# Performance work log

Measured on AMD Instinct MI355X. Metric: run time of the kernel, lower is better.

## Reference

```python
import jax, jax.numpy as jnp
import numpy as np

DIM = 1024
HEADS = 16

def setup_inputs() -> dict:
    key = jax.random.key(0)
    k1, k2, k3, k4 = jax.random.split(key, 4)
    x = jax.random.normal(k1, (2, 2048, DIM), dtype=jnp.float32)
    ln_gamma = jnp.ones((DIM,), dtype=jnp.float32)
    ln_beta = jnp.zeros((DIM,), dtype=jnp.float32)
    # torch Linear weight is [out, in]; store transposed [in, out] for x @ W
    W_qkv = jax.random.normal(k2, (DIM, 3 * DIM), dtype=jnp.float32) * (DIM ** -0.5)
    W_out = jax.random.normal(k3, (DIM, DIM), dtype=jnp.float32) * (DIM ** -0.5)
    b_out = jax.random.normal(k4, (DIM,), dtype=jnp.float32) * 0.02
    return {"x": x, "ln_gamma": ln_gamma, "ln_beta": ln_beta,
            "W_qkv": W_qkv, "W_out": W_out, "b_out": b_out}

def reference(x, ln_gamma, ln_beta, W_qkv, W_out, b_out):
    B, N, C = x.shape
    H = HEADS
    Dh = C // H
    scale = Dh ** -0.5
    # LayerNorm (eps=1e-5, torch default)
    mu = jnp.mean(x, axis=-1, keepdims=True)
    var = jnp.var(x, axis=-1, keepdims=True)
    xn = (x - mu) / jnp.sqrt(var + 1e-5) * ln_gamma + ln_beta
    # QKV projection: [B,N,3C] -> [3,B,H,N,Dh]
    qkv = (xn @ W_qkv).reshape(B, N, 3, H, Dh).transpose(2, 0, 3, 1, 4)
    q, k, v = qkv[0], qkv[1], qkv[2]
    attn = jnp.einsum('bhnd,bhmd->bhnm', q, k) * scale  # [B,H,N,N]
    attn = jax.nn.softmax(attn, axis=-1)
    out = jnp.einsum('bhnm,bhmd->bhnd', attn, v)  # [B,H,N,Dh]
    out = out.transpose(0, 2, 1, 3).reshape(B, N, C)
    return out @ W_out + b_out
```

## Files before the change

kernel.cpp:

```cpp
#include <hip/hip_runtime.h>
#include <hip/hip_bf16.h>

#define DIM 1024
#define HEADS 16
#define DH 64
#define SEQ 2048
#define BATCH 2
#define ROWS (BATCH*SEQ)
#define C3 (3*DIM)
#define NT (SEQ/64)

typedef __attribute__((ext_vector_type(8))) short s16x8;
typedef __attribute__((ext_vector_type(4))) short s16x4;
typedef __attribute__((ext_vector_type(4))) float f32x4;
typedef __attribute__((ext_vector_type(16))) float f32x16;
typedef __attribute__((ext_vector_type(4))) unsigned int u32x4;
typedef __attribute__((ext_vector_type(2))) unsigned int u32x2;

__device__ __forceinline__ void gll16(const void* g, void* l) {
  __builtin_amdgcn_global_load_lds((const __attribute__((address_space(1))) void*)g,
                                   (__attribute__((address_space(3))) void*)l, 16, 0, 0);
}
__device__ __forceinline__ float bf2f(short s) {
  return __builtin_bit_cast(float, ((unsigned)(unsigned short)s) << 16);
}
__device__ __forceinline__ short f2bf(float f) {
  return (short)__bfloat16_as_ushort(__float2bfloat16(f));
}
__device__ __forceinline__ unsigned pk2(float a, float b) {
  unsigned lo = (unsigned)__bfloat16_as_ushort(__float2bfloat16(a));
  unsigned hh = (unsigned)__bfloat16_as_ushort(__float2bfloat16(b));
  return lo | (hh << 16);
}
__device__ __forceinline__ float fexp2(float x) {
#if __has_builtin(__builtin_amdgcn_exp2f)
  return __builtin_amdgcn_exp2f(x);
#else
  float r; asm("v_exp_f32 %0, %1" : "=v"(r) : "v"(x)); return r;
#endif
}

__global__ __launch_bounds__(256) void prep_kernel(const float* __restrict__ x,
    const float* __restrict__ gamma, const float* __restrict__ beta,
    __hip_bfloat16* __restrict__ xn,
    const float* __restrict__ Wqkv, __hip_bfloat16* __restrict__ wqkv_t,
    const float* __restrict__ Wout, __hip_bfloat16* __restrict__ wout_t) {
  const int bid = blockIdx.x;
  const int t = threadIdx.x;
  if (bid < ROWS) {
    __shared__ float red[8];
    const float4* xp = (const float4*)(x + (size_t)bid * DIM);
    float4 v = xp[t];
    float s = v.x + v.y + v.z + v.w;
    float q = v.x*v.x + v.y*v.y + v.z*v.z + v.w*v.w;
    for (int off = 32; off >= 1; off >>= 1) {
      s += __shfl_xor(s, off, 64);
      q += __shfl_xor(q, off, 64);
    }
    int w = t >> 6;
    if ((t & 63) == 0) { red[w] = s; red[4 + w] = q; }
    __syncthreads();
    s = red[0] + red[1] + red[2] + red[3];
    q = red[4] + red[5] + red[6] + red[7];
    float mu = s * (1.0f / DIM);
    float var = q * (1.0f / DIM) - mu * mu;
    float rstd = rsqrtf(var + 1e-5f);
    float4 g4 = ((const float4*)gamma)[t];
    float4 b4 = ((const float4*)beta)[t];
    __hip_bfloat16* op = xn + (size_t)bid * DIM + t * 4;
    op[0] = __float2bfloat16((v.x - mu) * rstd * g4.x + b4.x);
    op[1] = __float2bfloat16((v.y - mu) * rstd * g4.y + b4.y);
    op[2] = __float2bfloat16((v.z - mu) * rstd * g4.z + b4.z);
    op[3] = __float2bfloat16((v.w - mu) * rstd * g4.w + b4.w);
  } else {
    __shared__ float tile[32][33];
    const float* in; __hip_bfloat16* out; int R, Cn, c0, r0;
    if (bid < ROWS + 3072) {
      int id = bid - ROWS;
      in = Wqkv; out = wqkv_t; R = DIM; Cn = C3;
      c0 = (id % 96) * 32; r0 = (id / 96) * 32;
    } else {
      int id = bid - ROWS - 3072;
      in = Wout; out = wout_t; R = DIM; Cn = DIM;
      c0 = (id % 32) * 32; r0 = (id / 32) * 32;
    }
    int tx = t & 31, ty = t >> 5;
#pragma unroll
    for (int i = 0; i < 4; i++)
      tile[ty + i * 8][tx] = in[(size_t)(r0 + ty + i * 8) * Cn + c0 + tx];
    __syncthreads();
#pragma unroll
    for (int i = 0; i < 4; i++)
      out[(size_t)(c0 + ty + i * 8) * R + r0 + tx] = __float2bfloat16(tile[tx][ty + i * 8]);
  }
}

__global__ __launch_bounds__(512) void gemm192(const __hip_bfloat16* __restrict__ A,
    const __hip_bfloat16* __restrict__ Bt, __hip_bfloat16* __restrict__ C,
    int M, int Nc, int K) {
  __shared__ short lds_a[2][256 * 64];
  __shared__ short lds_b[2][192 * 64];
  const int t = threadIdx.x, l = t & 63;
  const int w = t >> 6, wr = w >> 2, wc = w & 3;
  const int m0 = blockIdx.y * 256, n0 = blockIdx.x * 192;
  const short* Ab = (const short*)A;
  const short* Bb = (const short*)Bt;
  f32x4 acc[8][3] = {};
  const int srow = t >> 3;
  const int schk = (t & 7) ^ (srow & 7);
  const int NIT = K / 64;

  {
    char* la = (char*)&lds_a[0][0];
    char* lb = (char*)&lds_b[0][0];
#pragma unroll
    for (int p = 0; p < 4; p++)
      gll16(Ab + (size_t)(m0 + p * 64 + srow) * K + schk * 8, la + p * 8192 + t * 16);
#pragma unroll
    for (int p = 0; p < 3; p++)
      gll16(Bb + (size_t)(n0 + p * 64 + srow) * K + schk * 8, lb + p * 8192 + t * 16);
  }
  for (int it = 0; it < NIT; ++it) {
    const int cur = it & 1;
    __syncthreads();
    if (it + 1 < NIT) {
      const int kk = (it + 1) * 64;
      char* la = (char*)&lds_a[cur ^ 1][0];
      char* lb = (char*)&lds_b[cur ^ 1][0];
#pragma unroll
      for (int p = 0; p < 4; p++)
        gll16(Ab + (size_t)(m0 + p * 64 + srow) * K + kk + schk * 8, la + p * 8192 + t * 16);
#pragma unroll
      for (int p = 0; p < 3; p++)
        gll16(Bb + (size_t)(n0 + p * 64 + srow) * K + kk + schk * 8, lb + p * 8192 + t * 16);
      asm volatile("s_waitcnt vmcnt(7)" ::: "memory");
    } else {
      asm volatile("s_waitcnt vmcnt(0)" ::: "memory");
    }
    __syncthreads();
    const char* la = (const char*)&lds_a[cur][0];
    const char* lb = (const char*)&lds_b[cur][0];
    s16x8 af[4], bf[3];
#define GPH_READ_A(FH, S)                                                     \
    _Pragma("unroll")                                                         \
    for (int f = 0; f < 4; f++) {                                             \
      int row = wr * 128 + (FH * 4 + f) * 16 + (l & 15);                      \
      int chk = (((S) * 4 + (l >> 4)) ^ (l & 7)) * 16;                        \
      af[f] = *(const s16x8*)(la + row * 128 + chk);                          \
    }
#define GPH_READ_B(S)                                                         \
    _Pragma("unroll")                                                         \
    for (int n = 0; n < 3; n++) {                                             \
      int row = wc * 48 + n * 16 + (l & 15);                                  \
      int chk = (((S) * 4 + (l >> 4)) ^ (l & 7)) * 16;                        \
      bf[n] = *(const s16x8*)(lb + row * 128 + chk);                          \
    }
#define GPH_MFMA(FH)                                                          \
    __builtin_amdgcn_s_barrier();                                             \
    asm volatile("s_waitcnt lgkmcnt(0)" ::: "memory");                        \
    __builtin_amdgcn_sched_barrier(0);                                        \
    __builtin_amdgcn_s_setprio(1);                                            \
    _Pragma("unroll")                                                         \
    for (int f = 0; f < 4; f++)                                               \
      _Pragma("unroll")                                                       \
      for (int n = 0; n < 3; n++)                                             \
        acc[FH * 4 + f][n] =                                                  \
            __builtin_amdgcn_mfma_f32_16x16x32_bf16(af[f], bf[n],             \
                                                    acc[FH * 4 + f][n], 0, 0, 0); \
    __builtin_amdgcn_s_setprio(0);                                            \
    __builtin_amdgcn_s_barrier();

    GPH_READ_A(0, 0) GPH_READ_B(0) GPH_MFMA(0)
    GPH_READ_A(1, 0) GPH_MFMA(1)
    GPH_READ_A(0, 1) GPH_READ_B(1) GPH_MFMA(0)
    GPH_READ_A(1, 1) GPH_MFMA(1)
#undef GPH_READ_A
#undef GPH_READ_B
#undef GPH_MFMA
  }
#pragma unroll
  for (int f = 0; f < 8; f++)
#pragma unroll
    for (int n = 0; n < 3; n++) {
      int col = n0 + wc * 48 + n * 16 + (l & 15);
#pragma unroll
      for (int r = 0; r < 4; r++) {
        int row = m0 + wr * 128 + f * 16 + (l >> 4) * 4 + r;
        C[(size_t)row * Nc + col] = __float2bfloat16(acc[f][n][r]);
      }
    }
}

__global__ __launch_bounds__(256) void gemm_out(const __hip_bfloat16* __restrict__ A,
    const __hip_bfloat16* __restrict__ Bt, float* __restrict__ C,
    const float* __restrict__ bias) {
  __shared__ short lds_a[2][128 * 32];
  __shared__ short lds_b[2][64 * 32];
  const int t = threadIdx.x, l = t & 63, w = t >> 6;
  const int wr = w >> 1, wc = w & 1;
  const int m0 = blockIdx.y * 128, n0 = blockIdx.x * 64;
  const short* Ab = (const short*)A;
  const short* Bb = (const short*)Bt;
  const int K = DIM;
  f32x4 acc[4][2] = {};
  const int srow = t >> 2, scol = (t & 3) * 8;
  {
    char* la = (char*)&lds_a[0][0];
    char* lb = (char*)&lds_b[0][0];
    gll16(Ab + (size_t)(m0 + srow) * K + scol,      la + t * 16);
    gll16(Ab + (size_t)(m0 + 64 + srow) * K + scol, la + 4096 + t * 16);
    gll16(Bb + (size_t)(n0 + srow) * K + scol,      lb + t * 16);
  }
  for (int it = 0; it < K / 32; ++it) {
    const int cur = it & 1;
    __syncthreads();
    if (it + 1 < K / 32) {
      const int kk = (it + 1) * 32;
      char* la = (char*)&lds_a[cur ^ 1][0];
      char* lb = (char*)&lds_b[cur ^ 1][0];
      gll16(Ab + (size_t)(m0 + srow) * K + kk + scol,      la + t * 16);
      gll16(Ab + (size_t)(m0 + 64 + srow) * K + kk + scol, la + 4096 + t * 16);
      gll16(Bb + (size_t)(n0 + srow) * K + kk + scol,      lb + t * 16);
      asm volatile("s_waitcnt vmcnt(3)" ::: "memory");
    } else {
      asm volatile("s_waitcnt vmcnt(0)" ::: "memory");
    }
    __syncthreads();
    s16x8 af[4], bf[2];
#pragma unroll
    for (int m = 0; m < 4; m++)
      af[m] = *(const s16x8*)&lds_a[cur][(wr * 64 + m * 16 + (l & 15)) * 32 + (l >> 4) * 8];
#pragma unroll
    for (int n = 0; n < 2; n++)
      bf[n] = *(const s16x8*)&lds_b[cur][(wc * 32 + n * 16 + (l & 15)) * 32 + (l >> 4) * 8];
#pragma unroll
    for (int m = 0; m < 4; m++)
#pragma unroll
      for (int n = 0; n < 2; n++)
        acc[m][n] = __builtin_amdgcn_mfma_f32_16x16x32_bf16(af[m], bf[n], acc[m][n], 0, 0, 0);
  }
#pragma unroll
  for (int m = 0; m < 4; m++)
#pragma unroll
    for (int n = 0; n < 2; n++) {
      int col = n0 + wc * 32 + n * 16 + (l & 15);
      float bb = bias[col];
#pragma unroll
      for (int r = 0; r < 4; r++) {
        int row = m0 + wr * 64 + m * 16 + (l >> 4) * 4 + r;
        C[(size_t)row * DIM + col] = acc[m][n][r] + bb;
      }
    }
}

__global__ __launch_bounds__(512) void attn_kernel(const __hip_bfloat16* __restrict__ qkv,
    __hip_bfloat16* __restrict__ attno) {
  const int t = threadIdx.x, l = t & 63, w = t >> 6;
  const int hi = l >> 5, lq = l & 31;
  const int bid = blockIdx.x;
  const int xcd = bid & 7, j = bid >> 3;
  const int bh = xcd + 8 * (j & 3);
  const int qb = j >> 2;
  const int b = bh >> 4, h = bh & 15;
  const short* base  = (const short*)qkv + (size_t)b * SEQ * C3 + h * DH;
  const short* kbase = base + DIM;
  const short* vbase = base + 2 * DIM;
  const int qr0 = qb * 256 + w * 32;

  __shared__ short kbuf[2][2][64 * 64];
  __shared__ short vbuf[2][2][64 * 64];

  const float SCL = 0.125f * 1.44269504089f;
  s16x8 qf[4];
#pragma unroll
  for (int dk = 0; dk < 4; dk++) {
    s16x8 raw = *(const s16x8*)(base + (size_t)(qr0 + lq) * C3 + dk * 16 + hi * 8);
#pragma unroll
    for (int j2 = 0; j2 < 8; j2++) qf[dk][j2] = f2bf(bf2f(raw[j2]) * SCL);
  }

  s16x8 ones;
#pragma unroll
  for (int j2 = 0; j2 < 8; j2++) ones[j2] = (short)0x3F80;

  f32x16 o0, o1, osum, zf;
#pragma unroll
  for (int r = 0; r < 16; r++) { o0[r] = 0.f; o1[r] = 0.f; osum[r] = 0.f; zf[r] = 0.f; }
  asm volatile("" : "+v"(zf));

  const int krow = t >> 3;
  const int ksrc = (t & 7) ^ (krow & 7);
  const int vr = t & 31, vcg = t >> 5;

#define V_LOAD(VA, VB, ROW0)                                                    \
  VA = __builtin_bit_cast(u32x2, *(const s16x4*)(vbase + (size_t)((ROW0) + 2 * vr) * C3 + vcg * 4)); \
  VB = __builtin_bit_cast(u32x2, *(const s16x4*)(vbase + (size_t)((ROW0) + 2 * vr + 1) * C3 + vcg * 4));

#define V_WRITE(VD, VA, VB)                                                     \
  { char* vd_ = (char*)(VD);                                                    \
    _Pragma("unroll")                                                           \
    for (int i = 0; i < 4; i++) {                                               \
      int d = vcg * 4 + i;                                                      \
      unsigned dw = __builtin_amdgcn_perm((VB)[i >> 1], (VA)[i >> 1],           \
                                          (i & 1) ? 0x07060302u : 0x05040100u); \
      *(unsigned*)(vd_ + d * 128 + (((vr >> 2) ^ (d & 7)) * 16) + (vr & 3) * 4) = dw; } }

  {
    gll16(kbase + (size_t)krow * C3 + ksrc * 8,        (char*)&kbuf[0][0][0] + t * 16);
    gll16(kbase + (size_t)(64 + krow) * C3 + ksrc * 8, (char*)&kbuf[0][1][0] + t * 16);
    u32x2 va0, vb0, va1, vb1;
    V_LOAD(va0, vb0, 0)
    V_LOAD(va1, vb1, 64)
    V_WRITE(&vbuf[0][0][0], va0, vb0)
    V_WRITE(&vbuf[0][1][0], va1, vb1)
  }
  __syncthreads();

#define ATTN_SUB(KB, VB)                                                        \
  {                                                                             \
    const char* kb_ = (const char*)(KB);                                        \
    const char* vbp_ = (const char*)(VB);                                       \
    f32x16 st0, st1;                                                            \
    { int chk0 = (hi ^ (l & 7)) * 16;                                           \
      s16x8 kf0 = *(const s16x8*)(kb_ + (size_t)lq * 128 + chk0);               \
      s16x8 kf1 = *(const s16x8*)(kb_ + (size_t)(32 + lq) * 128 + chk0);        \
      st0 = __builtin_amdgcn_mfma_f32_32x32x16_bf16(kf0, qf[0], zf, 0, 0, 0);   \
      st1 = __builtin_amdgcn_mfma_f32_32x32x16_bf16(kf1, qf[0], zf, 0, 0, 0); } \
    _Pragma("unroll")                                                           \
    for (int dk = 1; dk < 4; dk++) {                                            \
      int chk = ((2 * dk + hi) ^ (l & 7)) * 16;                                 \
      s16x8 kf0 = *(const s16x8*)(kb_ + (size_t)lq * 128 + chk);                \
      s16x8 kf1 = *(const s16x8*)(kb_ + (size_t)(32 + lq) * 128 + chk);         \
      st0 = __builtin_amdgcn_mfma_f32_32x32x16_bf16(kf0, qf[dk], st0, 0, 0, 0); \
      st1 = __builtin_amdgcn_mfma_f32_32x32x16_bf16(kf1, qf[dk], st1, 0, 0, 0); \
    }                                                                           \
    _Pragma("unroll")                                                           \
    for (int r = 0; r < 16; r++) { st0[r] = fexp2(st0[r]); st1[r] = fexp2(st1[r]); } \
    _Pragma("unroll")                                                           \
    for (int n = 0; n < 2; n++) {                                               \
      const f32x16& stn = n ? st1 : st0;                                        \
      _Pragma("unroll")                                                         \
      for (int ksl = 0; ksl < 2; ksl++) {                                       \
        int rb = ksl * 8;                                                       \
        int a_ = (int)pk2(stn[rb + 0], stn[rb + 1]);                            \
        int b_ = (int)pk2(stn[rb + 2], stn[rb + 3]);                            \
        int c_ = (int)pk2(stn[rb + 4], stn[rb + 5]);                            \
        int d_ = (int)pk2(stn[rb + 6], stn[rb + 7]);                            \
        asm volatile("v_permlane32_swap_b32 %0, %1" : "+v"(a_), "+v"(c_));      \
        asm volatile("v_permlane32_swap_b32 %0, %1" : "+v"(b_), "+v"(d_));      \
        u32x4 fr;                                                               \
        fr.x = (unsigned)a_;  fr.y = (unsigned)b_;                              \
        fr.z = (unsigned)c_;  fr.w = (unsigned)d_;                              \
        s16x8 pa = __builtin_bit_cast(s16x8, fr);                               \
        int ks = n * 2 + ksl;                                                   \
        int chk = ((2 * ks + hi) ^ (l & 7)) * 16;                               \
        s16x8 vf0 = *(const s16x8*)(vbp_ + (size_t)lq * 128 + chk);             \
        s16x8 vf1 = *(const s16x8*)(vbp_ + (size_t)(32 + lq) * 128 + chk);      \
        o0   = __builtin_amdgcn_mfma_f32_32x32x16_bf16(pa, vf0, o0, 0, 0, 0);   \
        o1   = __builtin_amdgcn_mfma_f32_32x32x16_bf16(pa, vf1, o1, 0, 0, 0);   \
        osum = __builtin_amdgcn_mfma_f32_32x32x16_bf16(pa, ones, osum, 0, 0, 0);\
      }                                                                         \
    }                                                                           \
  }

  for (int it = 0; it < NT / 2; ++it) {
    const int cur = it & 1;
    const bool pf = (it + 1 < NT / 2);
    u32x2 va0, vb0, va1, vb1;
    if (pf) {
      const int kv1 = (it + 1) * 128;
      gll16(kbase + (size_t)(kv1 + krow) * C3 + ksrc * 8,      (char*)&kbuf[cur ^ 1][0][0] + t * 16);
      gll16(kbase + (size_t)(kv1 + 64 + krow) * C3 + ksrc * 8, (char*)&kbuf[cur ^ 1][1][0] + t * 16);
      V_LOAD(va0, vb0, kv1)
      V_LOAD(va1, vb1, kv1 + 64)
    }
    ATTN_SUB(&kbuf[cur][0][0], &vbuf[cur][0][0])
    ATTN_SUB(&kbuf[cur][1][0], &vbuf[cur][1][0])
    if (pf) {
      V_WRITE(&vbuf[cur ^ 1][0][0], va0, vb0)
      V_WRITE(&vbuf[cur ^ 1][1][0], va1, vb1)
    }
    __syncthreads();
  }
#undef ATTN_SUB
#undef V_LOAD
#undef V_WRITE

#pragma unroll
  for (int r = 0; r < 16; r++) {
    int qr = (r & 3) + 8 * (r >> 2) + 4 * hi;
    float ir = 1.0f / osum[r];
    size_t rowoff = (size_t)(b * SEQ + qr0 + qr) * DIM + h * DH;
    attno[rowoff + lq]      = __float2bfloat16(o0[r] * ir);
    attno[rowoff + 32 + lq] = __float2bfloat16(o1[r] * ir);
  }
}

extern "C" void kernel_launch(void* const* d_in, const int* in_sizes, int n_in,
                              void* d_out, int out_size, void* d_ws, size_t ws_size,
                              hipStream_t stream) {
  const float* x     = (const float*)d_in[0];
  const float* gamma = (const float*)d_in[1];
  const float* beta  = (const float*)d_in[2];
  const float* Wqkv  = (const float*)d_in[3];
  const float* Wout  = (const float*)d_in[4];
  const float* bout  = (const float*)d_in[5];

  __hip_bfloat16* xn     = (__hip_bfloat16*)d_ws;
  __hip_bfloat16* wqkv_t = xn + (size_t)ROWS * DIM;
  __hip_bfloat16* wout_t = wqkv_t + (size_t)C3 * DIM;
  __hip_bfloat16* qkv    = wout_t + (size_t)DIM * DIM;
  __hip_bfloat16* attno  = qkv + (size_t)ROWS * C3;

  prep_kernel<<<ROWS + 3072 + 1024, 256, 0, stream>>>(x, gamma, beta, xn,
                                                      Wqkv, wqkv_t, Wout, wout_t);
  gemm192<<<dim3(C3 / 192, ROWS / 256), 512, 0, stream>>>(xn, wqkv_t, qkv, ROWS, C3, DIM);
  attn_kernel<<<SEQ / 256 * BATCH * HEADS, 512, 0, stream>>>(qkv, attno);
  gemm_out<<<dim3(DIM / 64, ROWS / 128), 256, 0, stream>>>(attno, wout_t, (float*)d_out, bout);
}
```

Baseline: 119.8 us.

## Use 32x32 MFMA tiles in QKV GEMM and halve attention block size

The QKV GEMM switches from 16x16x32 to 32x32x16 MFMA with a 4x2 wave layout where each wave covers 64x96, so fewer LDS fragment reads are needed per FLOP. The attention kernel moves to 256-thread blocks covering 128 query rows, launching twice as many blocks, with wider 16-byte V loads and a K staging macro adjusted to the new thread count. The aim is to cut LDS traffic in the GEMM and improve occupancy and load balance in attention. The cost is more K/V staging per query row, since each KV tile is now shared by fewer queries.

```diff
diff --git a/kernel.cpp b/kernel.cpp
--- a/kernel.cpp
+++ b/kernel.cpp
@@ -101,11 +101,12 @@
   __shared__ short lds_a[2][256 * 64];
   __shared__ short lds_b[2][192 * 64];
   const int t = threadIdx.x, l = t & 63;
-  const int w = t >> 6, wr = w >> 2, wc = w & 3;
+  const int w = t >> 6, wr = w >> 1, wc = w & 1;
+  const int hi = l >> 5;
   const int m0 = blockIdx.y * 256, n0 = blockIdx.x * 192;
   const short* Ab = (const short*)A;
   const short* Bb = (const short*)Bt;
-  f32x4 acc[8][3] = {};
+  f32x16 acc[2][3] = {};
   const int srow = t >> 3;
   const int schk = (t & 7) ^ (srow & 7);
   const int NIT = K / 64;
@@ -140,53 +141,45 @@
     __syncthreads();
     const char* la = (const char*)&lds_a[cur][0];
     const char* lb = (const char*)&lds_b[cur][0];
-    s16x8 af[4], bf[3];
-#define GPH_READ_A(FH, S)                                                     \
-    _Pragma("unroll")                                                         \
-    for (int f = 0; f < 4; f++) {                                             \
-      int row = wr * 128 + (FH * 4 + f) * 16 + (l & 15);                      \
-      int chk = (((S) * 4 + (l >> 4)) ^ (l & 7)) * 16;                        \
-      af[f] = *(const s16x8*)(la + row * 128 + chk);                          \
-    }
-#define GPH_READ_B(S)                                                         \
-    _Pragma("unroll")                                                         \
-    for (int n = 0; n < 3; n++) {                                             \
-      int row = wc * 48 + n * 16 + (l & 15);                                  \
-      int chk = (((S) * 4 + (l >> 4)) ^ (l & 7)) * 16;                        \
-      bf[n] = *(const s16x8*)(lb + row * 128 + chk);                          \
-    }
-#define GPH_MFMA(FH)                                                          \
-    __builtin_amdgcn_s_barrier();                                             \
-    asm volatile("s_waitcnt lgkmcnt(0)" ::: "memory");                        \
-    __builtin_amdgcn_sched_barrier(0);                                        \
-    __builtin_amdgcn_s_setprio(1);                                            \
-    _Pragma("unroll")                                                         \
-    for (int f = 0; f < 4; f++)                                               \
-      _Pragma("unroll")                                                       \
-      for (int n = 0; n < 3; n++)                                             \
-        acc[FH * 4 + f][n] =                                                  \
-            __builtin_amdgcn_mfma_f32_16x16x32_bf16(af[f], bf[n],             \
-                                                    acc[FH * 4 + f][n], 0, 0, 0); \
-    __builtin_amdgcn_s_setprio(0);                                            \
-    __builtin_amdgcn_s_barrier();
-
-    GPH_READ_A(0, 0) GPH_READ_B(0) GPH_MFMA(0)
-    GPH_READ_A(1, 0) GPH_MFMA(1)
-    GPH_READ_A(0, 1) GPH_READ_B(1) GPH_MFMA(0)
-    GPH_READ_A(1, 1) GPH_MFMA(1)
-#undef GPH_READ_A
-#undef GPH_READ_B
-#undef GPH_MFMA
-  }
-#pragma unroll
-  for (int f = 0; f < 8; f++)
-#pragma unroll
-    for (int n = 0; n < 3; n++) {
-      int col = n0 + wc * 48 + n * 16 + (l & 15);
-#pragma unroll
-      for (int r = 0; r < 4; r++) {
-        int row = m0 + wr * 128 + f * 16 + (l >> 4) * 4 + r;
-        C[(size_t)row * Nc + col] = __float2bfloat16(acc[f][n][r]);
+#pragma unroll
+    for (int p = 0; p < 2; p++) {
+      s16x8 af[2][2], bf[2][3];
+#pragma unroll
+      for (int k2 = 0; k2 < 2; k2++) {
+        int g = 2 * (p * 2 + k2) + hi;
+        int chk = (g ^ (l & 7)) * 16;
+#pragma unroll
+        for (int rb = 0; rb < 2; rb++)
+          af[k2][rb] = *(const s16x8*)(la + (wr * 64 + rb * 32 + (l & 31)) * 128 + chk);
+#pragma unroll
+        for (int nn = 0; nn < 3; nn++)
+          bf[k2][nn] = *(const s16x8*)(lb + (wc * 96 + nn * 32 + (l & 31)) * 128 + chk);
+      }
+      __builtin_amdgcn_s_barrier();
+      asm volatile("s_waitcnt lgkmcnt(0)" ::: "memory");
+      __builtin_amdgcn_sched_barrier(0);
+      __builtin_amdgcn_s_setprio(1);
+#pragma unroll
+      for (int k2 = 0; k2 < 2; k2++)
+#pragma unroll
+        for (int rb = 0; rb < 2; rb++)
+#pragma unroll
+          for (int nn = 0; nn < 3; nn++)
+            acc[rb][nn] = __builtin_amdgcn_mfma_f32_32x32x16_bf16(
+                af[k2][rb], bf[k2][nn], acc[rb][nn], 0, 0, 0);
+      __builtin_amdgcn_s_setprio(0);
+      __builtin_amdgcn_s_barrier();
+    }
+  }
+#pragma unroll
+  for (int rb = 0; rb < 2; rb++)
+#pragma unroll
+    for (int nn = 0; nn < 3; nn++) {
+      int col = n0 + wc * 96 + nn * 32 + (l & 31);
+#pragma unroll
+      for (int r = 0; r < 16; r++) {
+        int row = m0 + wr * 64 + rb * 32 + (r & 3) + 8 * (r >> 2) + 4 * hi;
+        C[(size_t)row * Nc + col] = __float2bfloat16(acc[rb][nn][r]);
       }
     }
 }
@@ -253,7 +246,7 @@
     }
 }
 
-__global__ __launch_bounds__(512) void attn_kernel(const __hip_bfloat16* __restrict__ qkv,
+__global__ __launch_bounds__(256) void attn_kernel(const __hip_bfloat16* __restrict__ qkv,
     __hip_bfloat16* __restrict__ attno) {
   const int t = threadIdx.x, l = t & 63, w = t >> 6;
   const int hi = l >> 5, lq = l & 31;
@@ -265,7 +258,7 @@
   const short* base  = (const short*)qkv + (size_t)b * SEQ * C3 + h * DH;
   const short* kbase = base + DIM;
   const short* vbase = base + 2 * DIM;
-  const int qr0 = qb * 256 + w * 32;
+  const int qr0 = qb * 128 + w * 32;
 
   __shared__ short kbuf[2][2][64 * 64];
   __shared__ short vbuf[2][2][64 * 64];
@@ -290,25 +283,30 @@
 
   const int krow = t >> 3;
   const int ksrc = (t & 7) ^ (krow & 7);
-  const int vr = t & 31, vcg = t >> 5;
+  const int vr = t & 31, vc = (t >> 5) * 8;
+
+#define K_STAGE(DST, ROW0)                                                      \
+  { char* kd_ = (char*)(DST);                                                   \
+    gll16(kbase + (size_t)((ROW0) + krow) * C3 + ksrc * 8,      kd_ + t * 16);  \
+    gll16(kbase + (size_t)((ROW0) + 32 + krow) * C3 + ksrc * 8, kd_ + 4096 + t * 16); }
 
 #define V_LOAD(VA, VB, ROW0)                                                    \
-  VA = __builtin_bit_cast(u32x2, *(const s16x4*)(vbase + (size_t)((ROW0) + 2 * vr) * C3 + vcg * 4)); \
-  VB = __builtin_bit_cast(u32x2, *(const s16x4*)(vbase + (size_t)((ROW0) + 2 * vr + 1) * C3 + vcg * 4));
+  VA = __builtin_bit_cast(u32x4, *(const s16x8*)(vbase + (size_t)((ROW0) + 2 * vr) * C3 + vc)); \
+  VB = __builtin_bit_cast(u32x4, *(const s16x8*)(vbase + (size_t)((ROW0) + 2 * vr + 1) * C3 + vc));
 
 #define V_WRITE(VD, VA, VB)                                                     \
   { char* vd_ = (char*)(VD);                                                    \
     _Pragma("unroll")                                                           \
-    for (int i = 0; i < 4; i++) {                                               \
-      int d = vcg * 4 + i;                                                      \
+    for (int i = 0; i < 8; i++) {                                               \
+      int d = vc + i;                                                           \
       unsigned dw = __builtin_amdgcn_perm((VB)[i >> 1], (VA)[i >> 1],           \
                                           (i & 1) ? 0x07060302u : 0x05040100u); \
       *(unsigned*)(vd_ + d * 128 + (((vr >> 2) ^ (d & 7)) * 16) + (vr & 3) * 4) = dw; } }
 
   {
-    gll16(kbase + (size_t)krow * C3 + ksrc * 8,        (char*)&kbuf[0][0][0] + t * 16);
-    gll16(kbase + (size_t)(64 + krow) * C3 + ksrc * 8, (char*)&kbuf[0][1][0] + t * 16);
-    u32x2 va0, vb0, va1, vb1;
+    K_STAGE(&kbuf[0][0][0], 0)
+    K_STAGE(&kbuf[0][1][0], 64)
+    u32x4 va0, vb0, va1, vb1;
     V_LOAD(va0, vb0, 0)
     V_LOAD(va1, vb1, 64)
     V_WRITE(&vbuf[0][0][0], va0, vb0)
@@ -366,11 +364,11 @@
   for (int it = 0; it < NT / 2; ++it) {
     const int cur = it & 1;
     const bool pf = (it + 1 < NT / 2);
-    u32x2 va0, vb0, va1, vb1;
+    u32x4 va0, vb0, va1, vb1;
     if (pf) {
       const int kv1 = (it + 1) * 128;
-      gll16(kbase + (size_t)(kv1 + krow) * C3 + ksrc * 8,      (char*)&kbuf[cur ^ 1][0][0] + t * 16);
-      gll16(kbase + (size_t)(kv1 + 64 + krow) * C3 + ksrc * 8, (char*)&kbuf[cur ^ 1][1][0] + t * 16);
+      K_STAGE(&kbuf[cur ^ 1][0][0], kv1)
+      K_STAGE(&kbuf[cur ^ 1][1][0], kv1 + 64)
       V_LOAD(va0, vb0, kv1)
       V_LOAD(va1, vb1, kv1 + 64)
     }
@@ -383,6 +381,7 @@
     __syncthreads();
   }
 #undef ATTN_SUB
+#undef K_STAGE
 #undef V_LOAD
 #undef V_WRITE
 
@@ -415,6 +414,6 @@
   prep_kernel<<<ROWS + 3072 + 1024, 256, 0, stream>>>(x, gamma, beta, xn,
                                                       Wqkv, wqkv_t, Wout, wout_t);
   gemm192<<<dim3(C3 / 192, ROWS / 256), 512, 0, stream>>>(xn, wqkv_t, qkv, ROWS, C3, DIM);
-  attn_kernel<<<SEQ / 256 * BATCH * HEADS, 512, 0, stream>>>(qkv, attno);
+  attn_kernel<<<16 * BATCH * HEADS, 256, 0, stream>>>(qkv, attno);
   gemm_out<<<dim3(DIM / 64, ROWS / 128), 256, 0, stream>>>(attno, wout_t, (float*)d_out, bout);
 }
```

Result: slower. 124.6 us (+4.0%).
